# Kernel tuning notes

Measured on AMD Instinct MI355X. Metric: run time of the kernel, lower is better.

Reference implementation:

```python
import jax, jax.numpy as jnp
import numpy as np
from jax import lax

BATCH = 8192
DIM = 2048
NUM_STATES = 3


def setup_inputs() -> dict:
    key = jax.random.key(0)
    k1, k2, k3, k4 = jax.random.split(key, 4)
    y = jax.random.randint(k1, (BATCH, DIM), 0, 2, dtype=jnp.int64 if jax.config.jax_enable_x64 else jnp.int32)
    transition_probs = jax.random.normal(k2, (NUM_STATES, NUM_STATES), dtype=jnp.float32)
    emission_probs = jax.random.normal(k3, (NUM_STATES, 2), dtype=jnp.float32)
    start_probs = jax.random.normal(k4, (NUM_STATES,), dtype=jnp.float32)
    return {
        "y": y,
        "transition_probs": transition_probs,
        "emission_probs": emission_probs,
        "start_probs": start_probs,
    }


def reference(y, transition_probs, emission_probs, start_probs):
    # Normalize parameters in log space (matches torch.log_softmax)
    log_T = jax.nn.log_softmax(transition_probs, axis=-1)   # [S, S]
    log_E = jax.nn.log_softmax(emission_probs, axis=-1)     # [S, 2]
    log_pi = jax.nn.log_softmax(start_probs, axis=-1)       # [S]

    # Gather per-timestep emission log-probs: [B, DIM, S]
    em = log_E.T[y]

    # alpha_0[b, s] = log_pi[s] + log_E[s, y[b,0]]
    alpha0 = log_pi[None, :] + em[:, 0]                      # [B, S]

    def step(alpha, em_t):
        # alpha[b, i] + log_T[i, j] -> logsumexp over i, plus emission at t
        new = jax.nn.logsumexp(alpha[:, :, None] + log_T[None, :, :], axis=1) + em_t
        return new, None

    # Scan over time: em[:, 1:] moved to leading time axis -> [DIM-1, B, S]
    alpha_T, _ = lax.scan(step, alpha0, jnp.moveaxis(em[:, 1:], 1, 0))

    log_prob = jax.nn.logsumexp(alpha_T, axis=-1)            # [B]
    return log_prob.mean()
```

## Files before the change

kernel.cpp:

```cpp
#include <hip/hip_runtime.h>
#include <math.h>

#define BATCH 8192
#define DIM   2048

__global__ __launch_bounds__(256, 4)
void hmm_fwd(const int* __restrict__ y,
             const float* __restrict__ tp,
             const float* __restrict__ ep,
             const float* __restrict__ sp,
             float* __restrict__ row_lp,
             float* __restrict__ out_atomic)
{
    __shared__ float tbl[24 * 9];

    const int tid  = threadIdx.x;
    const int lane = tid & 63;
    const int wid  = tid >> 6;
    const int b    = blockIdx.x * 4 + wid;

    float T[3][3], E[3][2], pi[3];
    #pragma unroll
    for (int i = 0; i < 3; ++i) {
        float a0 = tp[i*3+0], a1 = tp[i*3+1], a2 = tp[i*3+2];
        float mx = fmaxf(a0, fmaxf(a1, a2));
        float e0 = __expf(a0-mx), e1 = __expf(a1-mx), e2 = __expf(a2-mx);
        float inv = 1.0f / (e0+e1+e2);
        T[i][0] = e0*inv; T[i][1] = e1*inv; T[i][2] = e2*inv;
    }
    #pragma unroll
    for (int s = 0; s < 3; ++s) {
        float a0 = ep[s*2+0], a1 = ep[s*2+1];
        float mx = fmaxf(a0, a1);
        float e0 = __expf(a0-mx), e1 = __expf(a1-mx);
        float inv = 1.0f / (e0+e1);
        E[s][0] = e0*inv; E[s][1] = e1*inv;
    }
    {
        float a0 = sp[0], a1 = sp[1], a2 = sp[2];
        float mx = fmaxf(a0, fmaxf(a1, a2));
        float e0 = __expf(a0-mx), e1 = __expf(a1-mx), e2 = __expf(a2-mx);
        float inv = 1.0f / (e0+e1+e2);
        pi[0] = e0*inv; pi[1] = e1*inv; pi[2] = e2*inv;
    }

    float M0[9], M1[9];
    #pragma unroll
    for (int k = 0; k < 3; ++k)
        #pragma unroll
        for (int j = 0; j < 3; ++j) {
            M0[k*3+j] = T[k][j] * E[j][0];
            M1[k*3+j] = T[k][j] * E[j][1];
        }

    if (tid < 24) {
        int code, n;
        if (tid < 16) { code = tid;      n = 4; }
        else          { code = tid - 16; n = 3; }
        float A[9];
        {
            const float* F = (code & 1) ? M1 : M0;
            #pragma unroll
            for (int e = 0; e < 9; ++e) A[e] = F[e];
            code >>= 1;
        }
        for (int s = 1; s < n; ++s) {
            const float* F = (code & 1) ? M1 : M0;
            code >>= 1;
            float Z[9];
            #pragma unroll
            for (int i = 0; i < 3; ++i)
                #pragma unroll
                for (int j = 0; j < 3; ++j)
                    Z[i*3+j] = fmaf(A[i*3+0], F[0*3+j],
                               fmaf(A[i*3+1], F[1*3+j], A[i*3+2]*F[2*3+j]));
            #pragma unroll
            for (int e = 0; e < 9; ++e) A[e] = Z[e];
        }
        #pragma unroll
        for (int e = 0; e < 9; ++e) tbl[tid*9 + e] = A[e];
    }
    __syncthreads();

    const int* __restrict__ yb = y + (size_t)b * DIM + lane * 32;

    float R[9] = {1.f,0.f,0.f, 0.f,1.f,0.f, 0.f,0.f,1.f};
    float lsc = 0.0f;
    int y0 = 0;

    #pragma unroll
    for (int g = 0; g < 8; ++g) {
        int4 q = *reinterpret_cast<const int4*>(yb + 4*g);
        int idx;
        if (g == 0) {
            y0 = q.x;
            int i4 = q.x + 2*q.y + 4*q.z + 8*q.w;
            int i3 = 16 + (q.y + 2*q.z + 4*q.w);
            idx = (lane == 0) ? i3 : i4;
        } else {
            idx = q.x + 2*q.y + 4*q.z + 8*q.w;
        }
        const float* __restrict__ G = &tbl[idx * 9];
        float g0 = G[0], g1 = G[1], g2 = G[2],
              g3 = G[3], g4 = G[4], g5 = G[5],
              g6 = G[6], g7 = G[7], g8 = G[8];
        float nR[9];
        #pragma unroll
        for (int i = 0; i < 3; ++i) {
            nR[i*3+0] = fmaf(R[i*3+0], g0, fmaf(R[i*3+1], g3, R[i*3+2]*g6));
            nR[i*3+1] = fmaf(R[i*3+0], g1, fmaf(R[i*3+1], g4, R[i*3+2]*g7));
            nR[i*3+2] = fmaf(R[i*3+0], g2, fmaf(R[i*3+1], g5, R[i*3+2]*g8));
        }
        #pragma unroll
        for (int e = 0; e < 9; ++e) R[e] = nR[e];

        if (g == 3 || g == 7) {
            float m = R[0];
            #pragma unroll
            for (int e = 1; e < 9; ++e) m = fmaxf(m, R[e]);
            lsc += __logf(m);
            float inv = 1.0f / m;
            #pragma unroll
            for (int e = 0; e < 9; ++e) R[e] *= inv;
        }
    }

    #pragma unroll
    for (int o = 1; o < 64; o <<= 1) {
        float S[9];
        #pragma unroll
        for (int e = 0; e < 9; ++e) S[e] = __shfl_down(R[e], o, 64);
        float osc = __shfl_down(lsc, o, 64);
        float nR[9];
        #pragma unroll
        for (int i = 0; i < 3; ++i)
            #pragma unroll
            for (int j = 0; j < 3; ++j)
                nR[i*3+j] = fmaf(R[i*3+0], S[0*3+j],
                            fmaf(R[i*3+1], S[1*3+j], R[i*3+2]*S[2*3+j]));
        #pragma unroll
        for (int e = 0; e < 9; ++e) R[e] = nR[e];
        lsc += osc;
    }

    if (lane == 0) {
        float e0 = y0 ? E[0][1] : E[0][0];
        float e1 = y0 ? E[1][1] : E[1][0];
        float e2 = y0 ? E[2][1] : E[2][0];
        float a0 = pi[0] * e0, a1 = pi[1] * e1, a2 = pi[2] * e2;
        float p = 0.0f;
        #pragma unroll
        for (int j = 0; j < 3; ++j)
            p += fmaf(a0, R[0*3+j], fmaf(a1, R[1*3+j], a2 * R[2*3+j]));
        float lp = __logf(p) + lsc;
        if (row_lp) row_lp[b] = lp;
        else        atomicAdd(out_atomic, lp * (1.0f / BATCH));
    }
}

__global__ void reduce_mean(const float* __restrict__ row, float* __restrict__ out)
{
    float s = 0.0f;
    for (int i = threadIdx.x; i < BATCH; i += 256) s += row[i];
    #pragma unroll
    for (int o = 32; o > 0; o >>= 1) s += __shfl_down(s, o, 64);
    __shared__ float sm[4];
    int w = threadIdx.x >> 6;
    if ((threadIdx.x & 63) == 0) sm[w] = s;
    __syncthreads();
    if (threadIdx.x == 0) out[0] = (sm[0] + sm[1] + sm[2] + sm[3]) * (1.0f / BATCH);
}

extern "C" void kernel_launch(void* const* d_in, const int* in_sizes, int n_in,
                              void* d_out, int out_size, void* d_ws, size_t ws_size,
                              hipStream_t stream)
{
    const int*   y  = (const int*)d_in[0];
    const float* tp = (const float*)d_in[1];
    const float* ep = (const float*)d_in[2];
    const float* sp = (const float*)d_in[3];
    float* out = (float*)d_out;

    const bool use_ws = (ws_size >= BATCH * sizeof(float));
    if (use_ws) {
        float* row = (float*)d_ws;
        hmm_fwd<<<BATCH/4, 256, 0, stream>>>(y, tp, ep, sp, row, nullptr);
        reduce_mean<<<1, 256, 0, stream>>>(row, out);
    } else {
        hipMemsetAsync(out, 0, sizeof(float), stream);
        hmm_fwd<<<BATCH/4, 256, 0, stream>>>(y, tp, ep, sp, nullptr, out);
    }
}
```

Baseline: 109.1 us.

## Coalesce y loads via LDS staging and use 8-step transfer-matrix table

Each wave now loads its y row with coalesced int4 loads (consecutive lanes read consecutive 16-byte chunks) and reshuffles them through a swizzled LDS stage, so each lane still gets its own contiguous 32-element chunk. The lookup table grows from 4-step to 8-step products (256 entries padded to 12 floats for float4 reads), which halves the per-lane matrix products. The first step is folded algebraically by pre-multiplying pi by the inverse of T. The reduce kernel is also widened to 1024 threads. Costs are larger LDS use (about 44KB per block), which may cut occupancy, an extra barrier, and possible numerical issues if T is near singular.

```diff
diff --git a/kernel.cpp b/kernel.cpp
--- a/kernel.cpp
+++ b/kernel.cpp
@@ -12,12 +12,20 @@
              float* __restrict__ row_lp,
              float* __restrict__ out_atomic)
 {
-    __shared__ float tbl[24 * 9];
+    __shared__ __align__(16) float t4[16 * 12];
+    __shared__ __align__(16) float t8[256 * 12];
+    __shared__ __align__(16) int   ystage[4][DIM];
 
     const int tid  = threadIdx.x;
     const int lane = tid & 63;
     const int wid  = tid >> 6;
     const int b    = blockIdx.x * 4 + wid;
+
+    const int* __restrict__ yb = y + (size_t)b * DIM;
+    int4 ld[8];
+    #pragma unroll
+    for (int g = 0; g < 8; ++g)
+        ld[g] = *reinterpret_cast<const int4*>(yb + g * 256 + lane * 4);
 
     float T[3][3], E[3][2], pi[3];
     #pragma unroll
@@ -44,6 +52,24 @@
         pi[0] = e0*inv; pi[1] = e1*inv; pi[2] = e2*inv;
     }
 
+    float v0, v1, v2;
+    {
+        float c00 =  (T[1][1]*T[2][2] - T[1][2]*T[2][1]);
+        float c01 = -(T[1][0]*T[2][2] - T[1][2]*T[2][0]);
+        float c02 =  (T[1][0]*T[2][1] - T[1][1]*T[2][0]);
+        float c10 = -(T[0][1]*T[2][2] - T[0][2]*T[2][1]);
+        float c11 =  (T[0][0]*T[2][2] - T[0][2]*T[2][0]);
+        float c12 = -(T[0][0]*T[2][1] - T[0][1]*T[2][0]);
+        float c20 =  (T[0][1]*T[1][2] - T[0][2]*T[1][1]);
+        float c21 = -(T[0][0]*T[1][2] - T[0][2]*T[1][0]);
+        float c22 =  (T[0][0]*T[1][1] - T[0][1]*T[1][0]);
+        float det = T[0][0]*c00 + T[0][1]*c01 + T[0][2]*c02;
+        float invd = 1.0f / det;
+        v0 = (pi[0]*c00 + pi[1]*c01 + pi[2]*c02) * invd;
+        v1 = (pi[0]*c10 + pi[1]*c11 + pi[2]*c12) * invd;
+        v2 = (pi[0]*c20 + pi[1]*c21 + pi[2]*c22) * invd;
+    }
+
     float M0[9], M1[9];
     #pragma unroll
     for (int k = 0; k < 3; ++k)
@@ -53,18 +79,14 @@
             M1[k*3+j] = T[k][j] * E[j][1];
         }
 
-    if (tid < 24) {
-        int code, n;
-        if (tid < 16) { code = tid;      n = 4; }
-        else          { code = tid - 16; n = 3; }
+    if (tid < 16) {
+        int code = tid;
         float A[9];
-        {
-            const float* F = (code & 1) ? M1 : M0;
-            #pragma unroll
-            for (int e = 0; e < 9; ++e) A[e] = F[e];
-            code >>= 1;
-        }
-        for (int s = 1; s < n; ++s) {
+        const float* F0 = (code & 1) ? M1 : M0;
+        #pragma unroll
+        for (int e = 0; e < 9; ++e) A[e] = F0[e];
+        code >>= 1;
+        for (int s = 1; s < 4; ++s) {
             const float* F = (code & 1) ? M1 : M0;
             code >>= 1;
             float Z[9];
@@ -78,32 +100,54 @@
             for (int e = 0; e < 9; ++e) A[e] = Z[e];
         }
         #pragma unroll
-        for (int e = 0; e < 9; ++e) tbl[tid*9 + e] = A[e];
+        for (int e = 0; e < 9; ++e) t4[tid*12 + e] = A[e];
+        t4[tid*12 +  9] = 0.0f; t4[tid*12 + 10] = 0.0f; t4[tid*12 + 11] = 0.0f;
     }
     __syncthreads();
-
-    const int* __restrict__ yb = y + (size_t)b * DIM + lane * 32;
+    {
+        const float* A = &t4[(tid & 15) * 12];
+        const float* B = &t4[(tid >> 4) * 12];
+        float Z[9];
+        #pragma unroll
+        for (int i = 0; i < 3; ++i)
+            #pragma unroll
+            for (int j = 0; j < 3; ++j)
+                Z[i*3+j] = fmaf(A[i*3+0], B[0*3+j],
+                           fmaf(A[i*3+1], B[1*3+j], A[i*3+2]*B[2*3+j]));
+        #pragma unroll
+        for (int e = 0; e < 9; ++e) t8[tid*12 + e] = Z[e];
+        t8[tid*12 +  9] = 0.0f; t8[tid*12 + 10] = 0.0f; t8[tid*12 + 11] = 0.0f;
+    }
+
+    #pragma unroll
+    for (int g = 0; g < 8; ++g) {
+        int Lp = 8*g + (lane >> 3);
+        int m  = lane & 7;
+        int off = Lp*32 + ((m ^ (Lp & 7)) * 4);
+        *reinterpret_cast<int4*>(&ystage[wid][off]) = ld[g];
+    }
+    __syncthreads();
+
+    int4 q[8];
+    #pragma unroll
+    for (int k = 0; k < 8; ++k) {
+        int off = lane*32 + ((k ^ (lane & 7)) * 4);
+        q[k] = *reinterpret_cast<const int4*>(&ystage[wid][off]);
+    }
 
     float R[9] = {1.f,0.f,0.f, 0.f,1.f,0.f, 0.f,0.f,1.f};
     float lsc = 0.0f;
-    int y0 = 0;
-
-    #pragma unroll
-    for (int g = 0; g < 8; ++g) {
-        int4 q = *reinterpret_cast<const int4*>(yb + 4*g);
-        int idx;
-        if (g == 0) {
-            y0 = q.x;
-            int i4 = q.x + 2*q.y + 4*q.z + 8*q.w;
-            int i3 = 16 + (q.y + 2*q.z + 4*q.w);
-            idx = (lane == 0) ? i3 : i4;
-        } else {
-            idx = q.x + 2*q.y + 4*q.z + 8*q.w;
-        }
-        const float* __restrict__ G = &tbl[idx * 9];
-        float g0 = G[0], g1 = G[1], g2 = G[2],
-              g3 = G[3], g4 = G[4], g5 = G[5],
-              g6 = G[6], g7 = G[7], g8 = G[8];
+
+    #pragma unroll
+    for (int j = 0; j < 4; ++j) {
+        int4 a = q[2*j], c = q[2*j+1];
+        int idx = a.x + (a.y<<1) + (a.z<<2) + (a.w<<3)
+                + (c.x<<4) + (c.y<<5) + (c.z<<6) + (c.w<<7);
+        const float4* G4 = reinterpret_cast<const float4*>(&t8[idx * 12]);
+        float4 p0 = G4[0], p1 = G4[1], p2 = G4[2];
+        float g0 = p0.x, g1 = p0.y, g2 = p0.z,
+              g3 = p0.w, g4 = p1.x, g5 = p1.y,
+              g6 = p1.z, g7 = p1.w, g8 = p2.x;
         float nR[9];
         #pragma unroll
         for (int i = 0; i < 3; ++i) {
@@ -114,7 +158,7 @@
         #pragma unroll
         for (int e = 0; e < 9; ++e) R[e] = nR[e];
 
-        if (g == 3 || g == 7) {
+        if (j == 1 || j == 3) {
             float m = R[0];
             #pragma unroll
             for (int e = 1; e < 9; ++e) m = fmaxf(m, R[e]);
@@ -144,14 +188,10 @@
     }
 
     if (lane == 0) {
-        float e0 = y0 ? E[0][1] : E[0][0];
-        float e1 = y0 ? E[1][1] : E[1][0];
-        float e2 = y0 ? E[2][1] : E[2][0];
-        float a0 = pi[0] * e0, a1 = pi[1] * e1, a2 = pi[2] * e2;
-        float p = 0.0f;
-        #pragma unroll
-        for (int j = 0; j < 3; ++j)
-            p += fmaf(a0, R[0*3+j], fmaf(a1, R[1*3+j], a2 * R[2*3+j]));
+        float r0 = R[0] + R[1] + R[2];
+        float r1 = R[3] + R[4] + R[5];
+        float r2 = R[6] + R[7] + R[8];
+        float p  = fmaf(v0, r0, fmaf(v1, r1, v2 * r2));
         float lp = __logf(p) + lsc;
         if (row_lp) row_lp[b] = lp;
         else        atomicAdd(out_atomic, lp * (1.0f / BATCH));
@@ -161,14 +201,19 @@
 __global__ void reduce_mean(const float* __restrict__ row, float* __restrict__ out)
 {
     float s = 0.0f;
-    for (int i = threadIdx.x; i < BATCH; i += 256) s += row[i];
+    for (int i = threadIdx.x; i < BATCH; i += 1024) s += row[i];
     #pragma unroll
     for (int o = 32; o > 0; o >>= 1) s += __shfl_down(s, o, 64);
-    __shared__ float sm[4];
+    __shared__ float sm[16];
     int w = threadIdx.x >> 6;
     if ((threadIdx.x & 63) == 0) sm[w] = s;
     __syncthreads();
-    if (threadIdx.x == 0) out[0] = (sm[0] + sm[1] + sm[2] + sm[3]) * (1.0f / BATCH);
+    if (threadIdx.x == 0) {
+        float t = 0.0f;
+        #pragma unroll
+        for (int i = 0; i < 16; ++i) t += sm[i];
+        out[0] = t * (1.0f / BATCH);
+    }
 }
 
 extern "C" void kernel_launch(void* const* d_in, const int* in_sizes, int n_in,
@@ -185,7 +230,7 @@
     if (use_ws) {
         float* row = (float*)d_ws;
         hmm_fwd<<<BATCH/4, 256, 0, stream>>>(y, tp, ep, sp, row, nullptr);
-        reduce_mean<<<1, 256, 0, stream>>>(row, out);
+        reduce_mean<<<1, 1024, 0, stream>>>(row, out);
     } else {
         hipMemsetAsync(out, 0, sizeof(float), stream);
         hmm_fwd<<<BATCH/4, 256, 0, stream>>>(y, tp, ep, sp, nullptr, out);
```

New measurement: 123.0 us. +12.7%, slower.
